# Kernel optimization log

Measured on AMD Instinct MI355X. Metric: run time of the kernel, lower is better.

The kernel has to match this reference:

```python
import jax, jax.numpy as jnp
import numpy as np

POOL_H, POOL_W = 7, 7
NUM_LEVELS = 4


def _crop_and_resize(image, boxes, box_indices, pool_h, pool_w):
    """Faithful tf.image.crop_and_resize (bilinear, extrapolation_value=0).

    image: [B, H, W, C]; boxes: [M, 4] (y1,x1,y2,x2) normalized; box_indices: [M] int32.
    Returns [M, pool_h, pool_w, C].
    """
    H, W = image.shape[1], image.shape[2]
    dt = image.dtype
    y1, x1, y2, x2 = boxes[:, 0], boxes[:, 1], boxes[:, 2], boxes[:, 3]
    gi = jnp.arange(pool_h, dtype=dt)
    gj = jnp.arange(pool_w, dtype=dt)
    # sample coordinates in source-image pixel space: [M, ph] / [M, pw]
    in_y = y1[:, None] * (H - 1) + gi[None, :] * ((y2 - y1) * (H - 1) / (pool_h - 1))[:, None]
    in_x = x1[:, None] * (W - 1) + gj[None, :] * ((x2 - x1) * (W - 1) / (pool_w - 1))[:, None]
    valid_y = (in_y >= 0) & (in_y <= H - 1)
    valid_x = (in_x >= 0) & (in_x <= W - 1)
    fy = jnp.floor(in_y)
    fx = jnp.floor(in_x)
    ty = jnp.clip(fy, 0, H - 1).astype(jnp.int32)
    by = jnp.minimum(ty + 1, H - 1)
    lx = jnp.clip(fx, 0, W - 1).astype(jnp.int32)
    rx = jnp.minimum(lx + 1, W - 1)
    wy = (in_y - fy)[:, :, None, None]   # [M, ph, 1, 1]
    wx = (in_x - fx)[:, None, :, None]   # [M, 1, pw, 1]
    bi = box_indices[:, None, None]
    tl = image[bi, ty[:, :, None], lx[:, None, :]]  # [M, ph, pw, C]
    tr = image[bi, ty[:, :, None], rx[:, None, :]]
    bl = image[bi, by[:, :, None], lx[:, None, :]]
    br = image[bi, by[:, :, None], rx[:, None, :]]
    top = tl + (tr - tl) * wx
    bot = bl + (br - bl) * wx
    out = top + (bot - top) * wy
    mask = (valid_y[:, :, None] & valid_x[:, None, :])[..., None]
    return jnp.where(mask, out, jnp.zeros((), dt))


def setup_inputs() -> dict:
    key = jax.random.key(0)
    ks = jax.random.split(key, 8)
    B, N, C = 2, 1000, 256
    sizes = [256, 128, 64, 32]
    yx1 = jax.random.uniform(ks[0], (B, N, 2), dtype=jnp.float32) * 0.8
    hw = jax.random.uniform(ks[1], (B, N, 2), dtype=jnp.float32) * 0.2 + 0.02
    boxes = jnp.concatenate([yx1, jnp.clip(yx1 + hw, 0.0, 1.0)], axis=-1)  # (y1,x1,y2,x2)
    fms = [jax.random.normal(ks[2 + l], (B, s, s, C), dtype=jnp.float32) for l, s in enumerate(sizes)]
    box_fpn_level = jax.random.randint(ks[6], (B, N), 1, NUM_LEVELS + 1, dtype=jnp.int32)
    return {"boxes": boxes, "fm0": fms[0], "fm1": fms[1], "fm2": fms[2], "fm3": fms[3],
            "box_fpn_level": box_fpn_level}


def reference(boxes, fm0, fm1, fm2, fm3, box_fpn_level):
    feature_maps = [fm0, fm1, fm2, fm3]
    B, N = boxes.shape[0], boxes.shape[1]
    C = fm0.shape[-1]
    flat_boxes = boxes.reshape(B * N, 4)
    flat_level = box_fpn_level.reshape(B * N)
    batch_idx = (jnp.arange(B * N, dtype=jnp.int32) // N).astype(jnp.int32)
    pooled = jnp.zeros((B * N, POOL_H, POOL_W, C), dtype=fm0.dtype)
    for l, fm in enumerate(feature_maps):
        p = _crop_and_resize(fm, flat_boxes, batch_idx, POOL_H, POOL_W)
        sel = (flat_level == l + 1)[:, None, None, None]
        pooled = jnp.where(sel, p, pooled)
    pooled = pooled.reshape(B, N, POOL_H, POOL_W, C)
    # TF concatenates per-level crops then dynamic_partitions by batch: within
    # each batch, boxes end up grouped by FPN level (stable within a level).
    order = jnp.argsort(box_fpn_level, axis=1, stable=True)  # [B, N]
    out = jnp.take_along_axis(pooled, order[:, :, None, None, None], axis=1)
    return out  # [B, MAX_OUTPUT_SIZE(=N), ph, pw, C]
```

## Files before the change

### kernel.cpp

```cpp
#include <hip/hip_runtime.h>

#define POOL 7
#define PP   (POOL * POOL)

__global__ void compute_order_kernel(const int* __restrict__ levels,
                                     int* __restrict__ dst, int N) {
    __shared__ int lvl[1024];
    const int b = blockIdx.x;
    const int n = threadIdx.x;
    const int* L = levels + (size_t)b * N;
    if (n < N) lvl[n] = L[n];
    __syncthreads();
    if (n < N) {
        const int my = lvl[n];
        int pos = 0;
        for (int m = 0; m < N; ++m) {
            const int lm = lvl[m];
            pos += (int)((lm < my) | ((lm == my) & (m < n)));
        }
        dst[(size_t)b * N + n] = pos;
    }
}

__global__ __launch_bounds__(64) void roi_align_kernel(
    const float* __restrict__ boxes,
    const float* __restrict__ fm0, const float* __restrict__ fm1,
    const float* __restrict__ fm2, const float* __restrict__ fm3,
    const int* __restrict__ levels, const int* __restrict__ dst,
    float* __restrict__ out, int N, int C) {

    const int box_flat = blockIdx.x;
    const int gi   = blockIdx.y;
    const int lane = threadIdx.x;
    const int b = box_flat / N;

    const int lv = levels[box_flat] - 1;
    const float* fm; int S;
    if      (lv == 0) { fm = fm0; S = 256; }
    else if (lv == 1) { fm = fm1; S = 128; }
    else if (lv == 2) { fm = fm2; S = 64;  }
    else              { fm = fm3; S = 32;  }

    const double y1 = (double)boxes[(size_t)box_flat * 4 + 0];
    const double x1 = (double)boxes[(size_t)box_flat * 4 + 1];
    const double y2 = (double)boxes[(size_t)box_flat * 4 + 2];
    const double x2 = (double)boxes[(size_t)box_flat * 4 + 3];

    const double Hm1 = (double)(S - 1);
    const double sy = (y2 - y1) * Hm1 / (double)(POOL - 1);
    const double sx = (x2 - x1) * Hm1 / (double)(POOL - 1);

    const double in_y = y1 * Hm1 + (double)gi * sy;
    const bool vy = (in_y >= 0.0) && (in_y <= Hm1);
    const double fy = floor(in_y);
    const float  wy = (float)(in_y - fy);
    const int ty = (int)fmin(fmax(fy, 0.0), Hm1);
    const int by = min(ty + 1, S - 1);

    const float* fmb  = fm + (size_t)b * S * S * C;
    const float* rowT = fmb + (size_t)ty * S * C;
    const float* rowB = fmb + (size_t)by * S * C;

    const int pos = dst[box_flat];
    float* orow = out + (((size_t)b * N + pos) * PP + (size_t)gi * POOL) * C
                      + lane * 4;

    const double ox = x1 * Hm1;
    const int c = lane * 4;

#pragma unroll
    for (int gj = 0; gj < POOL; ++gj) {
        const double in_x = ox + (double)gj * sx;
        const bool valid = vy && (in_x >= 0.0) && (in_x <= Hm1);

        float4 o;
        if (valid) {
            const double fx = floor(in_x);
            const float  wx = (float)(in_x - fx);
            const int lx = (int)fmin(fmax(fx, 0.0), Hm1);
            const int rx = min(lx + 1, S - 1);

            const float4 tl = *(const float4*)(rowT + (size_t)lx * C + c);
            const float4 tr = *(const float4*)(rowT + (size_t)rx * C + c);
            const float4 bl = *(const float4*)(rowB + (size_t)lx * C + c);
            const float4 br = *(const float4*)(rowB + (size_t)rx * C + c);

            float top = tl.x + (tr.x - tl.x) * wx;
            float bot = bl.x + (br.x - bl.x) * wx;
            o.x = top + (bot - top) * wy;
            top = tl.y + (tr.y - tl.y) * wx;
            bot = bl.y + (br.y - bl.y) * wx;
            o.y = top + (bot - top) * wy;
            top = tl.z + (tr.z - tl.z) * wx;
            bot = bl.z + (br.z - bl.z) * wx;
            o.z = top + (bot - top) * wy;
            top = tl.w + (tr.w - tl.w) * wx;
            bot = bl.w + (br.w - bl.w) * wx;
            o.w = top + (bot - top) * wy;
        } else {
            o.x = 0.0f; o.y = 0.0f; o.z = 0.0f; o.w = 0.0f;
        }
        *(float4*)(orow + (size_t)gj * C) = o;
    }
}

extern "C" void kernel_launch(void* const* d_in, const int* in_sizes, int n_in,
                              void* d_out, int out_size, void* d_ws, size_t ws_size,
                              hipStream_t stream) {
    const float* boxes  = (const float*)d_in[0];
    const float* fm0    = (const float*)d_in[1];
    const float* fm1    = (const float*)d_in[2];
    const float* fm2    = (const float*)d_in[3];
    const float* fm3    = (const float*)d_in[4];
    const int*   levels = (const int*)d_in[5];
    float* out = (float*)d_out;

    const int BN = in_sizes[5];
    const int C  = out_size / (BN * PP);
    const int B  = in_sizes[1] / (256 * 256 * C);
    const int N  = BN / B;

    int* dst = (int*)d_ws;

    compute_order_kernel<<<B, 1024, 0, stream>>>(levels, dst, N);
    roi_align_kernel<<<dim3(BN, POOL), 64, 0, stream>>>(
        boxes, fm0, fm1, fm2, fm3, levels, dst, out, N, C);
}
```

Measured before the change: 300.1 us.

## Merge pool rows into one block per box and use nontemporal output stores

```diff
diff --git a/kernel.cpp b/kernel.cpp
--- a/kernel.cpp
+++ b/kernel.cpp
@@ -2,6 +2,8 @@
 
 #define POOL 7
 #define PP   (POOL * POOL)
+
+typedef float floatx4 __attribute__((ext_vector_type(4)));
 
 __global__ void compute_order_kernel(const int* __restrict__ levels,
                                      int* __restrict__ dst, int N) {
@@ -22,7 +24,7 @@
     }
 }
 
-__global__ __launch_bounds__(64) void roi_align_kernel(
+__global__ __launch_bounds__(448) void roi_align_kernel(
     const float* __restrict__ boxes,
     const float* __restrict__ fm0, const float* __restrict__ fm1,
     const float* __restrict__ fm2, const float* __restrict__ fm3,
@@ -30,8 +32,8 @@
     float* __restrict__ out, int N, int C) {
 
     const int box_flat = blockIdx.x;
-    const int gi   = blockIdx.y;
-    const int lane = threadIdx.x;
+    const int gi   = threadIdx.x >> 6;
+    const int lane = threadIdx.x & 63;
     const int b = box_flat / N;
 
     const int lv = levels[box_flat] - 1;
@@ -73,34 +75,25 @@
         const double in_x = ox + (double)gj * sx;
         const bool valid = vy && (in_x >= 0.0) && (in_x <= Hm1);
 
-        float4 o;
+        floatx4 o;
         if (valid) {
             const double fx = floor(in_x);
             const float  wx = (float)(in_x - fx);
             const int lx = (int)fmin(fmax(fx, 0.0), Hm1);
             const int rx = min(lx + 1, S - 1);
 
-            const float4 tl = *(const float4*)(rowT + (size_t)lx * C + c);
-            const float4 tr = *(const float4*)(rowT + (size_t)rx * C + c);
-            const float4 bl = *(const float4*)(rowB + (size_t)lx * C + c);
-            const float4 br = *(const float4*)(rowB + (size_t)rx * C + c);
+            const floatx4 tl = *(const floatx4*)(rowT + (size_t)lx * C + c);
+            const floatx4 tr = *(const floatx4*)(rowT + (size_t)rx * C + c);
+            const floatx4 bl = *(const floatx4*)(rowB + (size_t)lx * C + c);
+            const floatx4 br = *(const floatx4*)(rowB + (size_t)rx * C + c);
 
-            float top = tl.x + (tr.x - tl.x) * wx;
-            float bot = bl.x + (br.x - bl.x) * wx;
-            o.x = top + (bot - top) * wy;
-            top = tl.y + (tr.y - tl.y) * wx;
-            bot = bl.y + (br.y - bl.y) * wx;
-            o.y = top + (bot - top) * wy;
-            top = tl.z + (tr.z - tl.z) * wx;
-            bot = bl.z + (br.z - bl.z) * wx;
-            o.z = top + (bot - top) * wy;
-            top = tl.w + (tr.w - tl.w) * wx;
-            bot = bl.w + (br.w - bl.w) * wx;
-            o.w = top + (bot - top) * wy;
+            const floatx4 top = tl + (tr - tl) * wx;
+            const floatx4 bot = bl + (br - bl) * wx;
+            o = top + (bot - top) * wy;
         } else {
-            o.x = 0.0f; o.y = 0.0f; o.z = 0.0f; o.w = 0.0f;
+            o = (floatx4)0.0f;
         }
-        *(float4*)(orow + (size_t)gj * C) = o;
+        __builtin_nontemporal_store(o, (floatx4*)(orow + (size_t)gj * C));
     }
 }
 
@@ -123,6 +116,6 @@
     int* dst = (int*)d_ws;
 
     compute_order_kernel<<<B, 1024, 0, stream>>>(levels, dst, N);
-    roi_align_kernel<<<dim3(BN, POOL), 64, 0, stream>>>(
+    roi_align_kernel<<<BN, 448, 0, stream>>>(
         boxes, fm0, fm1, fm2, fm3, levels, dst, out, N, C);
 }
```

Result: no change. 297.9 us (-0.7%).
